# Performance work log

Hardware: AMD Instinct MI355X
Metric: run time of the kernel (lower is better)

## Reference

```python
import jax, jax.numpy as jnp
import numpy as np

TAU_S = 2.0  # fixed in the original module


def setup_inputs() -> dict:
    key = jax.random.key(0)
    T, N, C = 64, 512, 2048
    inputs = jax.random.normal(key, (T, N, C), dtype=jnp.float32)
    return {"inputs": inputs}


def reference(inputs):
    # syn_t = syn_{t-1} + (x_t - syn_{t-1}) / tau_s
    #       = syn_{t-1} * (1 - 1/tau) + x_t / tau, syn_{-1} = 0
    decay = jnp.asarray(1.0 - 1.0 / TAU_S, dtype=inputs.dtype)
    inv_tau = jnp.asarray(1.0 / TAU_S, dtype=inputs.dtype)

    def step(syn, x_t):
        syn = syn * decay + x_t * inv_tau
        return syn, syn

    syn0 = jnp.zeros(inputs.shape[1:], dtype=inputs.dtype)
    _, syns = jax.lax.scan(step, syn0, inputs)
    return syns  # (T, N, C)
```

## Files before the change

kernel.cpp:

```cpp
#include <hip/hip_runtime.h>


typedef float f4 __attribute__((ext_vector_type(4)));

#define NC4 (512 * 2048 / 4)
#define CHUNK 16
#define NCHUNK 4
#define COLS 64

__global__ __launch_bounds__(256) void psp_scan_kernel(
    const f4* __restrict__ in, f4* __restrict__ out) {
    const int col   = threadIdx.x & (COLS - 1);
    const int chunk = threadIdx.x >> 6;
    const int colIdx = blockIdx.x * COLS + col;

    const f4* ip = in  + (size_t)(chunk * CHUNK) * NC4 + colIdx;
    f4*       op = out + (size_t)(chunk * CHUNK) * NC4 + colIdx;

    f4 v[CHUNK];
#pragma unroll
    for (int j = 0; j < CHUNK; ++j)
        v[j] = ip[(size_t)j * NC4];

    f4 acc = {0.f, 0.f, 0.f, 0.f};
#pragma unroll
    for (int j = 0; j < CHUNK; ++j) {
        acc = 0.5f * (acc + v[j]);
        v[j] = acc;
    }

    __shared__ f4 finals[NCHUNK][COLS];
    finals[chunk][col] = acc;
    __syncthreads();

    f4 carry = {0.f, 0.f, 0.f, 0.f};
    if (chunk >= 1) carry = finals[chunk - 1][col];
    if (chunk >= 2) carry += finals[chunk - 2][col] * 0x1p-16f;
    if (chunk >= 3) carry += finals[chunk - 3][col] * 0x1p-32f;

    float d = 0.5f;
#pragma unroll
    for (int j = 0; j < CHUNK; ++j) {
        op[(size_t)j * NC4] = v[j] + carry * d;
        d *= 0.5f;
    }
}

extern "C" void kernel_launch(void* const* d_in, const int* in_sizes, int n_in,
                              void* d_out, int out_size, void* d_ws, size_t ws_size,
                              hipStream_t stream) {
    const f4* in = (const f4*)d_in[0];
    f4* out = (f4*)d_out;
    psp_scan_kernel<<<NC4 / COLS, 256, 0, stream>>>(in, out);
}
```

Measured before the change: 435.7 us.

## Stage time chunks through LDS with sequential per-column scan and swizzled blocks

Replaces the four-way chunked parallel scan with carry fixup by a block that owns 256 column vectors. The block loops over four 16-step chunks, staging each chunk through a 64KB shared tile, and each thread then runs the recurrence sequentially over all 64 timesteps. Block indices are remapped so that adjacent blocks are spread across eight groups of the column range. The change drops the decayed-carry combine and gives each wave contiguous 4KB row segments to load and store. In exchange it needs large LDS per block, which limits occupancy, and it adds two barriers per chunk that serialise load, compute and store phases.

```diff
diff --git a/kernel.cpp b/kernel.cpp
--- a/kernel.cpp
+++ b/kernel.cpp
@@ -6,43 +6,51 @@
 #define NC4 (512 * 2048 / 4)
 #define CHUNK 16
 #define NCHUNK 4
-#define COLS 64
+#define W 256
+#define NWIN (NC4 / W)
 
 __global__ __launch_bounds__(256) void psp_scan_kernel(
     const f4* __restrict__ in, f4* __restrict__ out) {
-    const int col   = threadIdx.x & (COLS - 1);
-    const int chunk = threadIdx.x >> 6;
-    const int colIdx = blockIdx.x * COLS + col;
+    const int bid = blockIdx.x;
+    const int win = (bid & 7) * (NWIN / 8) + (bid >> 3);
 
-    const f4* ip = in  + (size_t)(chunk * CHUNK) * NC4 + colIdx;
-    f4*       op = out + (size_t)(chunk * CHUNK) * NC4 + colIdx;
+    __shared__ f4 tile[CHUNK][W];
 
-    f4 v[CHUNK];
-#pragma unroll
-    for (int j = 0; j < CHUNK; ++j)
-        v[j] = ip[(size_t)j * NC4];
+    const int tid  = threadIdx.x;
+    const int wave = tid >> 6;
+    const int lane = tid & 63;
+    const size_t colBase = (size_t)win * W;
 
     f4 acc = {0.f, 0.f, 0.f, 0.f};
+
+    for (int c = 0; c < NCHUNK; ++c) {
+        const size_t base = (size_t)(c * CHUNK) * NC4 + colBase;
+
 #pragma unroll
-    for (int j = 0; j < CHUNK; ++j) {
-        acc = 0.5f * (acc + v[j]);
-        v[j] = acc;
-    }
+        for (int k = 0; k < 4; ++k) {
+            const int s = wave * 4 + k;
+            const f4* src = in + base + (size_t)s * NC4;
+#pragma unroll
+            for (int i = 0; i < W / 64; ++i)
+                tile[s][i * 64 + lane] = src[i * 64 + lane];
+        }
+        __syncthreads();
 
-    __shared__ f4 finals[NCHUNK][COLS];
-    finals[chunk][col] = acc;
-    __syncthreads();
+#pragma unroll
+        for (int t = 0; t < CHUNK; ++t) {
+            acc = 0.5f * (acc + tile[t][tid]);
+            tile[t][tid] = acc;
+        }
+        __syncthreads();
 
-    f4 carry = {0.f, 0.f, 0.f, 0.f};
-    if (chunk >= 1) carry = finals[chunk - 1][col];
-    if (chunk >= 2) carry += finals[chunk - 2][col] * 0x1p-16f;
-    if (chunk >= 3) carry += finals[chunk - 3][col] * 0x1p-32f;
-
-    float d = 0.5f;
 #pragma unroll
-    for (int j = 0; j < CHUNK; ++j) {
-        op[(size_t)j * NC4] = v[j] + carry * d;
-        d *= 0.5f;
+        for (int k = 0; k < 4; ++k) {
+            const int s = wave * 4 + k;
+            f4* dst = out + base + (size_t)s * NC4;
+#pragma unroll
+            for (int i = 0; i < W / 64; ++i)
+                dst[i * 64 + lane] = tile[s][i * 64 + lane];
+        }
     }
 }
 
@@ -51,5 +59,5 @@
                               hipStream_t stream) {
     const f4* in = (const f4*)d_in[0];
     f4* out = (f4*)d_out;
-    psp_scan_kernel<<<NC4 / COLS, 256, 0, stream>>>(in, out);
+    psp_scan_kernel<<<NWIN, 256, 0, stream>>>(in, out);
 }
```

Measured after the change: 439.3 us. Within noise of the previous version (+0.8%).

## Split time scan into four sequential chunk launches carrying state via output

Applied to the files above, without the earlier changes.

Replaces the single kernel, which combined chunk carries through shared memory, with four launches that each scan 16 timesteps. Each launch seeds its accumulator by reading the last output row of the previous chunk. Blocks are remapped with an interleaved window index so each launch touches a wide, contiguous column range. This removes the shared-memory carry fix-up and the barrier, at the cost of four kernel launches with serial dependencies and an extra read of one row per chunk.

```diff
diff --git a/kernel.cpp b/kernel.cpp
--- a/kernel.cpp
+++ b/kernel.cpp
@@ -5,45 +5,34 @@
 
 #define NC4 (512 * 2048 / 4)
 #define CHUNK 16
-#define NCHUNK 4
-#define COLS 64
+#define NBLK 1024
 
-__global__ __launch_bounds__(256) void psp_scan_kernel(
-    const f4* __restrict__ in, f4* __restrict__ out) {
-    const int col   = threadIdx.x & (COLS - 1);
-    const int chunk = threadIdx.x >> 6;
-    const int colIdx = blockIdx.x * COLS + col;
+__global__ __launch_bounds__(256) void psp_chunk_kernel(
+    const f4* __restrict__ in, f4* __restrict__ out, int t0) {
+    const int bid = blockIdx.x;
+    const int win = (bid & 7) * (NBLK / 8) + (bid >> 3);
+    const int col = win * 256 + (int)threadIdx.x;
 
-    const f4* ip = in  + (size_t)(chunk * CHUNK) * NC4 + colIdx;
-    f4*       op = out + (size_t)(chunk * CHUNK) * NC4 + colIdx;
+    const f4* ip = in  + (size_t)t0 * NC4 + col;
+    f4*       op = out + (size_t)t0 * NC4 + col;
+
+    f4 acc = {0.f, 0.f, 0.f, 0.f};
+    if (t0 > 0) acc = out[(size_t)(t0 - 1) * NC4 + col];
 
     f4 v[CHUNK];
 #pragma unroll
     for (int j = 0; j < CHUNK; ++j)
         v[j] = ip[(size_t)j * NC4];
 
-    f4 acc = {0.f, 0.f, 0.f, 0.f};
 #pragma unroll
     for (int j = 0; j < CHUNK; ++j) {
         acc = 0.5f * (acc + v[j]);
         v[j] = acc;
     }
 
-    __shared__ f4 finals[NCHUNK][COLS];
-    finals[chunk][col] = acc;
-    __syncthreads();
-
-    f4 carry = {0.f, 0.f, 0.f, 0.f};
-    if (chunk >= 1) carry = finals[chunk - 1][col];
-    if (chunk >= 2) carry += finals[chunk - 2][col] * 0x1p-16f;
-    if (chunk >= 3) carry += finals[chunk - 3][col] * 0x1p-32f;
-
-    float d = 0.5f;
 #pragma unroll
-    for (int j = 0; j < CHUNK; ++j) {
-        op[(size_t)j * NC4] = v[j] + carry * d;
-        d *= 0.5f;
-    }
+    for (int j = 0; j < CHUNK; ++j)
+        op[(size_t)j * NC4] = v[j];
 }
 
 extern "C" void kernel_launch(void* const* d_in, const int* in_sizes, int n_in,
@@ -51,5 +40,6 @@
                               hipStream_t stream) {
     const f4* in = (const f4*)d_in[0];
     f4* out = (f4*)d_out;
-    psp_scan_kernel<<<NC4 / COLS, 256, 0, stream>>>(in, out);
+    for (int c = 0; c < 4; ++c)
+        psp_chunk_kernel<<<NBLK, 256, 0, stream>>>(in, out, c * CHUNK);
 }
```

Result: slower. 444.9 us (+2.1%).
